# Optimization experiments

Hardware: AMD Instinct MI355X
Metric: run time of the kernel (lower is better)

Reference implementation:

```python
import jax, jax.numpy as jnp
import numpy as np

N_NODES = 50000
N_EDGES = 800000
IN_DIM = 1024
HID = 512          # hidden_channels * heads, heads=1
N_CLASSES = 6
N_GRAPHS = 8
NEG_SLOPE = 0.2    # PyG GATConv default LeakyReLU slope
EPS = 1e-16


def gat_conv(x, W, att_src, att_dst, bias, src, dst):
    """PyG GATConv with heads=1, concat=True.
    x: [N, Fin], W: [Fin, C], att_src/att_dst: [C], bias: [C],
    src/dst: [E] (edge_index[0], edge_index[1]); messages flow src -> dst.
    """
    h = x @ W                                   # [N, C]
    a_s = h @ att_src                           # [N]
    a_d = h @ att_dst                           # [N]
    e = jax.nn.leaky_relu(a_s[src] + a_d[dst], NEG_SLOPE)   # [E]
    # segment softmax over destination node
    m = jax.ops.segment_max(e, dst, num_segments=N_NODES)   # [N]
    ex = jnp.exp(e - m[dst])                                 # [E]
    denom = jax.ops.segment_sum(ex, dst, num_segments=N_NODES)  # [N]
    alpha = ex / (denom[dst] + EPS)                           # [E]
    msg = alpha[:, None] * h[src]                             # [E, C]
    out = jax.ops.segment_sum(msg, dst, num_segments=N_NODES)  # [N, C]
    return out + bias


def setup_inputs() -> dict:
    key = jax.random.key(0)
    ks = jax.random.split(key, 20)
    x = jax.random.normal(ks[0], (N_NODES, IN_DIM), dtype=jnp.float32)
    edge_index = jax.random.randint(ks[1], (2, N_EDGES), 0, N_NODES, dtype=jnp.int32)
    batch = jnp.sort(jax.random.randint(ks[2], (N_NODES,), 0, N_GRAPHS, dtype=jnp.int32))

    def glorot(k, shape):
        fan = shape[0] + shape[-1]
        return jax.random.normal(k, shape, dtype=jnp.float32) * jnp.sqrt(2.0 / fan)

    inp = {"x": x, "edge_index": edge_index, "batch": batch}
    dims = [(IN_DIM, HID), (HID, HID), (HID, HID)]
    for i, (fi, fo) in enumerate(dims, start=1):
        inp[f"W{i}"] = glorot(ks[3 * i], (fi, fo))
        inp[f"as{i}"] = glorot(ks[3 * i + 1], (fo,))
        inp[f"ad{i}"] = glorot(ks[3 * i + 2], (fo,))
        inp[f"b{i}"] = jnp.zeros((fo,), dtype=jnp.float32)
    inp["Wlin"] = glorot(ks[13], (HID, N_CLASSES))
    inp["blin"] = jnp.zeros((N_CLASSES,), dtype=jnp.float32)
    return inp


def reference(x, W1, as1, ad1, b1, W2, as2, ad2, b2, W3, as3, ad3, b3,
              Wlin, blin, edge_index, batch):
    src, dst = edge_index[0], edge_index[1]
    h = gat_conv(x, W1, as1, ad1, b1, src, dst)
    h = jax.nn.relu(h)
    h = gat_conv(h, W2, as2, ad2, b2, src, dst)
    h = jax.nn.relu(h)
    h = gat_conv(h, W3, as3, ad3, b3, src, dst)
    # global_max_pool over graphs; dropout is identity in eval mode
    pooled = jax.ops.segment_max(h, batch, num_segments=N_GRAPHS)  # [G, HID]
    return pooled @ Wlin + blin                                     # [G, num_classes]
```

## Files before the change

kernel.cpp:

```cpp
#include <hip/hip_runtime.h>
#include <cmath>

#define N_NODES 50000
#define N_EDGES 800000
#define IN_DIM 1024
#define HID 512
#define N_CLASSES 6
#define N_GRAPHS 8
#define NEG_SLOPE 0.2f
#define SCAN_BLK 256
#define N_SCAN_BLOCKS ((N_NODES + SCAN_BLK - 1) / SCAN_BLK)
#define POOL_STRIP 256
#define POOL_NBLOCKS ((N_NODES + POOL_STRIP - 1) / POOL_STRIP)

typedef _Float16 half8 __attribute__((ext_vector_type(8)));
typedef _Float16 half4 __attribute__((ext_vector_type(4)));
typedef float floatx4 __attribute__((ext_vector_type(4)));

__global__ __launch_bounds__(256) void transpose_cast_W(const float* __restrict__ W,
                                                        _Float16* __restrict__ Wt,
                                                        int K) {
    __shared__ float sh[32][33];
    const int kb = blockIdx.x * 32, nb = blockIdx.y * 32;
    const int tx = threadIdx.x & 31, ty = threadIdx.x >> 5;
#pragma unroll
    for (int i = 0; i < 32; i += 8)
        sh[ty + i][tx] = W[(size_t)(kb + ty + i) * HID + nb + tx];
    __syncthreads();
#pragma unroll
    for (int i = 0; i < 32; i += 8)
        Wt[(size_t)(nb + ty + i) * K + kb + tx] = (_Float16)sh[tx][ty + i];
}

template <typename AT>
__global__ __launch_bounds__(256) void gemm_mfma(const AT* __restrict__ A,
                                                 const _Float16* __restrict__ Bt,
                                                 _Float16* __restrict__ C,
                                                 int M, int K) {
    const int nwg = gridDim.x;
    const int bid = blockIdx.x;
    const int q = nwg >> 3, r = nwg & 7;
    const int xcd = bid & 7, local = bid >> 3;
    const int wgid = (xcd < r) ? xcd * (q + 1) + local
                               : r * (q + 1) + (xcd - r) * q + local;
    const int rowBase = (wgid >> 2) * 128;
    const int colBase = (wgid & 3) * 128;

    const int tid  = threadIdx.x;
    const int lane = tid & 63;
    const int wave = tid >> 6;
    const int wm = wave >> 1, wn = wave & 1;

    __shared__ _Float16 As[128][40];
    __shared__ _Float16 Bs[128][40];

    const int srow  = tid >> 1;
    const int shalf = (tid & 1) * 16;

    const int fr = lane & 15;
    const int kc = lane >> 4;

    floatx4 acc[4][4] = {};

    int arow = rowBase + srow; if (arow >= M) arow = M - 1;
    const AT*       aRow = A  + (size_t)arow * K + shalf;
    const _Float16* bRow = Bt + (size_t)(colBase + srow) * K + shalf;

    for (int kb = 0; kb < K; kb += 32) {
        half8* dstA = (half8*)&As[srow][shalf];
        half8* dstB = (half8*)&Bs[srow][shalf];
        if constexpr (sizeof(AT) == 4) {
            const float* ap = (const float*)aRow + kb;
            float4 af0 = *(const float4*)(ap + 0);
            float4 af1 = *(const float4*)(ap + 4);
            float4 af2 = *(const float4*)(ap + 8);
            float4 af3 = *(const float4*)(ap + 12);
            union { _Float16 h[16]; half8 v[2]; } au;
            au.h[0]  = (_Float16)af0.x; au.h[1]  = (_Float16)af0.y;
            au.h[2]  = (_Float16)af0.z; au.h[3]  = (_Float16)af0.w;
            au.h[4]  = (_Float16)af1.x; au.h[5]  = (_Float16)af1.y;
            au.h[6]  = (_Float16)af1.z; au.h[7]  = (_Float16)af1.w;
            au.h[8]  = (_Float16)af2.x; au.h[9]  = (_Float16)af2.y;
            au.h[10] = (_Float16)af2.z; au.h[11] = (_Float16)af2.w;
            au.h[12] = (_Float16)af3.x; au.h[13] = (_Float16)af3.y;
            au.h[14] = (_Float16)af3.z; au.h[15] = (_Float16)af3.w;
            dstA[0] = au.v[0]; dstA[1] = au.v[1];
        } else {
            const _Float16* ap = (const _Float16*)aRow + kb;
            half8 a0 = *(const half8*)ap;
            half8 a1 = *(const half8*)(ap + 8);
            dstA[0] = a0; dstA[1] = a1;
        }
        const _Float16* bp = bRow + kb;
        half8 b0 = *(const half8*)bp;
        half8 b1 = *(const half8*)(bp + 8);
        dstB[0] = b0; dstB[1] = b1;
        __syncthreads();

        half8 afr[4], bfr[4];
#pragma unroll
        for (int mi = 0; mi < 4; ++mi)
            afr[mi] = *(const half8*)&As[wm * 64 + mi * 16 + fr][kc * 8];
#pragma unroll
        for (int ni = 0; ni < 4; ++ni)
            bfr[ni] = *(const half8*)&Bs[wn * 64 + ni * 16 + fr][kc * 8];
#pragma unroll
        for (int mi = 0; mi < 4; ++mi)
#pragma unroll
            for (int ni = 0; ni < 4; ++ni)
                acc[mi][ni] = __builtin_amdgcn_mfma_f32_16x16x32_f16(
                    afr[mi], bfr[ni], acc[mi][ni], 0, 0, 0);
        __syncthreads();
    }

#pragma unroll
    for (int mi = 0; mi < 4; ++mi) {
#pragma unroll
        for (int ni = 0; ni < 4; ++ni) {
            int col = colBase + wn * 64 + ni * 16 + fr;
#pragma unroll
            for (int j = 0; j < 4; ++j) {
                int row = rowBase + wm * 64 + mi * 16 + kc * 4 + j;
                if (row < M) C[(size_t)row * HID + col] = (_Float16)acc[mi][ni][j];
            }
        }
    }
}

__global__ __launch_bounds__(256) void adot_kernel(const _Float16* __restrict__ h,
                                                   const float* __restrict__ att_s,
                                                   const float* __restrict__ att_d,
                                                   float* __restrict__ a_s,
                                                   float* __restrict__ a_d) {
    int wave = threadIdx.x >> 6;
    int lane = threadIdx.x & 63;
    int n = blockIdx.x * 4 + wave;
    if (n >= N_NODES) return;
    half8 hv = *(const half8*)(h + (size_t)n * HID + lane * 8);
    float4 s0 = ((const float4*)att_s)[lane * 2];
    float4 s1 = ((const float4*)att_s)[lane * 2 + 1];
    float4 d0 = ((const float4*)att_d)[lane * 2];
    float4 d1 = ((const float4*)att_d)[lane * 2 + 1];
    float hf[8];
#pragma unroll
    for (int q = 0; q < 8; ++q) hf[q] = (float)hv[q];
    float ss = hf[0]*s0.x + hf[1]*s0.y + hf[2]*s0.z + hf[3]*s0.w
             + hf[4]*s1.x + hf[5]*s1.y + hf[6]*s1.z + hf[7]*s1.w;
    float sd = hf[0]*d0.x + hf[1]*d0.y + hf[2]*d0.z + hf[3]*d0.w
             + hf[4]*d1.x + hf[5]*d1.y + hf[6]*d1.z + hf[7]*d1.w;
#pragma unroll
    for (int off = 32; off; off >>= 1) {
        ss += __shfl_down(ss, off);
        sd += __shfl_down(sd, off);
    }
    if (lane == 0) { a_s[n] = ss; a_d[n] = sd; }
}

__global__ void count_kernel(const int* __restrict__ dst, int* __restrict__ cnt) {
    int i = blockIdx.x * blockDim.x + threadIdx.x;
    if (i < N_EDGES) atomicAdd(cnt + dst[i], 1);
}

__global__ __launch_bounds__(SCAN_BLK) void scan1_kernel(const int* __restrict__ cnt,
                                                         int* __restrict__ partial,
                                                         int* __restrict__ blocksum) {
    __shared__ int tmp[SCAN_BLK];
    int t = threadIdx.x;
    int i = blockIdx.x * SCAN_BLK + t;
    int v = (i < N_NODES) ? cnt[i] : 0;
    tmp[t] = v;
    __syncthreads();
    for (int off = 1; off < SCAN_BLK; off <<= 1) {
        int u = (t >= off) ? tmp[t - off] : 0;
        __syncthreads();
        tmp[t] += u;
        __syncthreads();
    }
    if (i < N_NODES) partial[i] = tmp[t] - v;
    if (t == SCAN_BLK - 1) blocksum[blockIdx.x] = tmp[t];
}

__global__ __launch_bounds__(SCAN_BLK) void scan2_kernel(int* __restrict__ blocksum) {
    __shared__ int tmp[SCAN_BLK];
    int t = threadIdx.x;
    int v = (t < N_SCAN_BLOCKS) ? blocksum[t] : 0;
    tmp[t] = v;
    __syncthreads();
    for (int off = 1; off < SCAN_BLK; off <<= 1) {
        int u = (t >= off) ? tmp[t - off] : 0;
        __syncthreads();
        tmp[t] += u;
        __syncthreads();
    }
    if (t < N_SCAN_BLOCKS) blocksum[t] = tmp[t] - v;
}

__global__ __launch_bounds__(SCAN_BLK) void scan3_kernel(const int* __restrict__ partial,
                                                         const int* __restrict__ blocksum,
                                                         int* __restrict__ rowptr,
                                                         int* __restrict__ cursor) {
    int i = blockIdx.x * SCAN_BLK + threadIdx.x;
    if (i < N_NODES) {
        int r = partial[i] + blocksum[blockIdx.x];
        rowptr[i] = r;
        cursor[i] = r;
    }
    if (i == 0) rowptr[N_NODES] = N_EDGES;
}

__global__ void scatter_kernel(const int* __restrict__ src, const int* __restrict__ dst,
                               int* __restrict__ cursor, int* __restrict__ src_s) {
    int i = blockIdx.x * blockDim.x + threadIdx.x;
    if (i >= N_EDGES) return;
    int p = atomicAdd(cursor + dst[i], 1);
    src_s[p] = src[i];
}

__global__ __launch_bounds__(256) void aggregate_fused(const int* __restrict__ rowptr,
                                                       const int* __restrict__ src_s,
                                                       const float* __restrict__ a_s,
                                                       const float* __restrict__ a_d,
                                                       const _Float16* __restrict__ h,
                                                       const float* __restrict__ bias,
                                                       int do_relu,
                                                       _Float16* __restrict__ outx) {
    int wave = threadIdx.x >> 6;
    int lane = threadIdx.x & 63;
    int n = blockIdx.x * 4 + wave;
    if (n >= N_NODES) return;
    int beg = rowptr[n], end = rowptr[n + 1];
    float a_dn = a_d[n];
    float m = -__builtin_inff();
    float ssum = 0.f;
    float acc[8] = {};
    for (int j = beg; j < end; ++j) {
        int s = src_s[j];
        float v = a_s[s] + a_dn;
        v = v > 0.f ? v : NEG_SLOPE * v;
        float mn = fmaxf(m, v);
        float scale = __expf(m - mn);
        float p = __expf(v - mn);
        ssum = ssum * scale + p;
        m = mn;
        half8 hv = *(const half8*)(h + (size_t)s * HID + lane * 8);
#pragma unroll
        for (int q = 0; q < 8; ++q)
            acc[q] = fmaf(p, (float)hv[q], acc[q] * scale);
    }
    float inv = 1.f / (ssum + 1e-16f);
    const float4 b0 = ((const float4*)(bias + lane * 8))[0];
    const float4 b1 = ((const float4*)(bias + lane * 8))[1];
    float o[8];
    o[0] = acc[0] * inv + b0.x; o[1] = acc[1] * inv + b0.y;
    o[2] = acc[2] * inv + b0.z; o[3] = acc[3] * inv + b0.w;
    o[4] = acc[4] * inv + b1.x; o[5] = acc[5] * inv + b1.y;
    o[6] = acc[6] * inv + b1.z; o[7] = acc[7] * inv + b1.w;
    half8 ov;
#pragma unroll
    for (int q = 0; q < 8; ++q) {
        float val = do_relu ? fmaxf(o[q], 0.f) : o[q];
        ov[q] = (_Float16)val;
    }
    *(half8*)(outx + (size_t)n * HID + lane * 8) = ov;
}

__global__ __launch_bounds__(128) void pool1_kernel(const _Float16* __restrict__ X,
                                                    const int* __restrict__ batch,
                                                    float* __restrict__ partial) {
    const int t = threadIdx.x;
    const int b = blockIdx.x;
    const int n0 = b * POOL_STRIP;
    const int n1 = min(n0 + POOL_STRIP, N_NODES);
    const float NEG = -__builtin_inff();
    const float4 neg4 = make_float4(NEG, NEG, NEG, NEG);
#pragma unroll
    for (int g = 0; g < N_GRAPHS; ++g)
        ((float4*)(partial + ((size_t)b * N_GRAPHS + g) * HID))[t] = neg4;
    int gcur = batch[n0];
    float4 m = neg4;
    for (int n = n0; n < n1; ++n) {
        int g = batch[n];
        if (g != gcur) {
            ((float4*)(partial + ((size_t)b * N_GRAPHS + gcur) * HID))[t] = m;
            m = neg4;
            gcur = g;
        }
        half4 hv = *(const half4*)(X + (size_t)n * HID + t * 4);
        m.x = fmaxf(m.x, (float)hv[0]); m.y = fmaxf(m.y, (float)hv[1]);
        m.z = fmaxf(m.z, (float)hv[2]); m.w = fmaxf(m.w, (float)hv[3]);
    }
    ((float4*)(partial + ((size_t)b * N_GRAPHS + gcur) * HID))[t] = m;
}

__global__ __launch_bounds__(128) void pool2_kernel(const float* __restrict__ partial,
                                                    float* __restrict__ pooled) {
    const int g = blockIdx.x;
    const int t = threadIdx.x;
    const float NEG = -__builtin_inff();
    float4 m = make_float4(NEG, NEG, NEG, NEG);
    for (int b = 0; b < POOL_NBLOCKS; ++b) {
        float4 v = ((const float4*)(partial + ((size_t)b * N_GRAPHS + g) * HID))[t];
        m.x = fmaxf(m.x, v.x); m.y = fmaxf(m.y, v.y);
        m.z = fmaxf(m.z, v.z); m.w = fmaxf(m.w, v.w);
    }
    ((float4*)(pooled + (size_t)g * HID))[t] = m;
}

__global__ __launch_bounds__(64) void final_linear_kernel(const float* __restrict__ pooled,
                                                          const float* __restrict__ Wlin,
                                                          const float* __restrict__ blin,
                                                          float* __restrict__ out) {
    int t = threadIdx.x;
    if (t >= N_GRAPHS * N_CLASSES) return;
    int g = t / N_CLASSES, c = t % N_CLASSES;
    float s = blin[c];
    for (int k = 0; k < HID; ++k)
        s = fmaf(pooled[(size_t)g * HID + k], Wlin[(size_t)k * N_CLASSES + c], s);
    out[t] = s;
}

extern "C" void kernel_launch(void* const* d_in, const int* in_sizes, int n_in,
                              void* d_out, int out_size, void* d_ws, size_t ws_size,
                              hipStream_t stream) {
    const float* x       = (const float*)d_in[0];
    const int*   eidx    = (const int*)d_in[1];
    const int*   batch   = (const int*)d_in[2];
    const float* W[3]    = {(const float*)d_in[3], (const float*)d_in[7], (const float*)d_in[11]};
    const float* Asrc[3] = {(const float*)d_in[4], (const float*)d_in[8], (const float*)d_in[12]};
    const float* Adst[3] = {(const float*)d_in[5], (const float*)d_in[9], (const float*)d_in[13]};
    const float* Bias[3] = {(const float*)d_in[6], (const float*)d_in[10], (const float*)d_in[14]};
    const float* Wlin    = (const float*)d_in[15];
    const float* blin    = (const float*)d_in[16];
    const int* src = eidx;
    const int* dst = eidx + N_EDGES;

    float* bufH   = (float*)d_ws;
    float* bufX   = bufH + (size_t)N_NODES * HID;
    float* a_s    = bufX + (size_t)N_NODES * HID;
    float* a_d    = a_s + N_NODES;
    float* pooled = a_d + N_NODES;
    int* cnt      = (int*)(pooled + N_GRAPHS * HID);
    int* rowptr   = cnt + N_NODES;
    int* cursor   = rowptr + N_NODES + 1;
    int* partial  = cursor + N_NODES;
    int* blocksum = partial + N_NODES;
    int* src_s    = blocksum + 256;
    _Float16* Wt  = (_Float16*)(src_s + N_EDGES);
    _Float16* hH  = (_Float16*)bufH;
    _Float16* xAct= (_Float16*)bufX;

    int edge_blocks = (N_EDGES + 255) / 256;

    hipMemsetAsync(cnt, 0, N_NODES * sizeof(int), stream);
    count_kernel<<<edge_blocks, 256, 0, stream>>>(dst, cnt);
    scan1_kernel<<<N_SCAN_BLOCKS, SCAN_BLK, 0, stream>>>(cnt, partial, blocksum);
    scan2_kernel<<<1, SCAN_BLK, 0, stream>>>(blocksum);
    scan3_kernel<<<N_SCAN_BLOCKS, SCAN_BLK, 0, stream>>>(partial, blocksum, rowptr, cursor);
    scatter_kernel<<<edge_blocks, 256, 0, stream>>>(src, dst, cursor, src_s);

    const int nrow_tiles = (N_NODES + 127) / 128;
    const int gemm_blocks = nrow_tiles * (HID / 128);
    for (int l = 0; l < 3; ++l) {
        int K = (l == 0) ? IN_DIM : HID;
        dim3 tgrid(K / 32, HID / 32);
        transpose_cast_W<<<tgrid, 256, 0, stream>>>(W[l], Wt, K);
        if (l == 0)
            gemm_mfma<float><<<gemm_blocks, 256, 0, stream>>>(x, Wt, hH, N_NODES, K);
        else
            gemm_mfma<_Float16><<<gemm_blocks, 256, 0, stream>>>(xAct, Wt, hH, N_NODES, K);
        adot_kernel<<<(N_NODES + 3) / 4, 256, 0, stream>>>(hH, Asrc[l], Adst[l], a_s, a_d);
        aggregate_fused<<<(N_NODES + 3) / 4, 256, 0, stream>>>(
            rowptr, src_s, a_s, a_d, hH, Bias[l], (l < 2) ? 1 : 0, xAct);
    }

    float* pool_partial = bufH;
    pool1_kernel<<<POOL_NBLOCKS, 128, 0, stream>>>(xAct, batch, pool_partial);
    pool2_kernel<<<N_GRAPHS, 128, 0, stream>>>(pool_partial, pooled);
    final_linear_kernel<<<1, 64, 0, stream>>>(pooled, Wlin, blin, (float*)d_out);
}
```

Before: 881.2 us.

## Double-buffer GEMM shared-memory tiles with register prefetch of next K-slice

The MFMA GEMM now keeps two shared-memory buffers for the A and B tiles. Each iteration issues the global loads for the next K-slice into registers before running the MFMAs on the current buffer, then writes that slice into the other buffer. This cuts the synchronisations per iteration from two to one and lets global-memory latency overlap with compute. The cost is double the LDS footprint and more live registers, which could lower occupancy.

```diff
diff --git a/kernel.cpp b/kernel.cpp
--- a/kernel.cpp
+++ b/kernel.cpp
@@ -51,8 +51,8 @@
     const int wave = tid >> 6;
     const int wm = wave >> 1, wn = wave & 1;
 
-    __shared__ _Float16 As[128][40];
-    __shared__ _Float16 Bs[128][40];
+    __shared__ _Float16 As[2][128][40];
+    __shared__ _Float16 Bs[2][128][40];
 
     const int srow  = tid >> 1;
     const int shalf = (tid & 1) * 16;
@@ -66,16 +66,16 @@
     const AT*       aRow = A  + (size_t)arow * K + shalf;
     const _Float16* bRow = Bt + (size_t)(colBase + srow) * K + shalf;
 
-    for (int kb = 0; kb < K; kb += 32) {
-        half8* dstA = (half8*)&As[srow][shalf];
-        half8* dstB = (half8*)&Bs[srow][shalf];
+    union { _Float16 h[16]; half8 v[2]; } au;
+    half8 bv0, bv1;
+
+    auto load_tile = [&](int kb) {
         if constexpr (sizeof(AT) == 4) {
             const float* ap = (const float*)aRow + kb;
             float4 af0 = *(const float4*)(ap + 0);
             float4 af1 = *(const float4*)(ap + 4);
             float4 af2 = *(const float4*)(ap + 8);
             float4 af3 = *(const float4*)(ap + 12);
-            union { _Float16 h[16]; half8 v[2]; } au;
             au.h[0]  = (_Float16)af0.x; au.h[1]  = (_Float16)af0.y;
             au.h[2]  = (_Float16)af0.z; au.h[3]  = (_Float16)af0.w;
             au.h[4]  = (_Float16)af1.x; au.h[5]  = (_Float16)af1.y;
@@ -84,33 +84,50 @@
             au.h[10] = (_Float16)af2.z; au.h[11] = (_Float16)af2.w;
             au.h[12] = (_Float16)af3.x; au.h[13] = (_Float16)af3.y;
             au.h[14] = (_Float16)af3.z; au.h[15] = (_Float16)af3.w;
-            dstA[0] = au.v[0]; dstA[1] = au.v[1];
         } else {
             const _Float16* ap = (const _Float16*)aRow + kb;
-            half8 a0 = *(const half8*)ap;
-            half8 a1 = *(const half8*)(ap + 8);
-            dstA[0] = a0; dstA[1] = a1;
+            au.v[0] = *(const half8*)ap;
+            au.v[1] = *(const half8*)(ap + 8);
         }
         const _Float16* bp = bRow + kb;
-        half8 b0 = *(const half8*)bp;
-        half8 b1 = *(const half8*)(bp + 8);
-        dstB[0] = b0; dstB[1] = b1;
-        __syncthreads();
+        bv0 = *(const half8*)bp;
+        bv1 = *(const half8*)(bp + 8);
+    };
+    auto store_tile = [&](int buf) {
+        half8* dstA = (half8*)&As[buf][srow][shalf];
+        half8* dstB = (half8*)&Bs[buf][srow][shalf];
+        dstA[0] = au.v[0]; dstA[1] = au.v[1];
+        dstB[0] = bv0;     dstB[1] = bv1;
+    };
+
+    load_tile(0);
+    store_tile(0);
+    __syncthreads();
+
+    int cur = 0;
+    for (int kb = 0; kb < K; kb += 32) {
+        const bool has_next = (kb + 32) < K;
+        if (has_next) load_tile(kb + 32);
 
         half8 afr[4], bfr[4];
 #pragma unroll
         for (int mi = 0; mi < 4; ++mi)
-            afr[mi] = *(const half8*)&As[wm * 64 + mi * 16 + fr][kc * 8];
+            afr[mi] = *(const half8*)&As[cur][wm * 64 + mi * 16 + fr][kc * 8];
 #pragma unroll
         for (int ni = 0; ni < 4; ++ni)
-            bfr[ni] = *(const half8*)&Bs[wn * 64 + ni * 16 + fr][kc * 8];
+            bfr[ni] = *(const half8*)&Bs[cur][wn * 64 + ni * 16 + fr][kc * 8];
 #pragma unroll
         for (int mi = 0; mi < 4; ++mi)
 #pragma unroll
             for (int ni = 0; ni < 4; ++ni)
                 acc[mi][ni] = __builtin_amdgcn_mfma_f32_16x16x32_f16(
                     afr[mi], bfr[ni], acc[mi][ni], 0, 0, 0);
-        __syncthreads();
+
+        if (has_next) {
+            store_tile(cur ^ 1);
+            __syncthreads();
+            cur ^= 1;
+        }
     }
 
 #pragma unroll
```

Result: slower. 940.1 us (+6.7%).

## Use direct global-to-LDS loads with swizzled 64-wide K tiles in GEMM

Applied to the files above, without the earlier changes.

Adds a separate pass that casts x to fp16 up front, so one fp16 GEMM kernel serves all three layers. The GEMM now fills LDS with global_load_lds 16-byte copies into an XOR-swizzled 128x64 layout, doubling the K step and halving the number of barriers. This removes the register round trip and the in-loop fp32 conversion. The cost is an extra full read and write of x, and the workspace offsets are rearranged to hold the fp16 copy.

```diff
diff --git a/kernel.cpp b/kernel.cpp
--- a/kernel.cpp
+++ b/kernel.cpp
@@ -17,6 +17,28 @@
 typedef _Float16 half4 __attribute__((ext_vector_type(4)));
 typedef float floatx4 __attribute__((ext_vector_type(4)));
 
+typedef const __attribute__((address_space(1))) void* gas_ptr;
+typedef __attribute__((address_space(3))) void* las_ptr;
+#define GLOAD16(gp, lp) \
+    __builtin_amdgcn_global_load_lds((gas_ptr)(gp), (las_ptr)(lp), 16, 0, 0)
+
+__global__ __launch_bounds__(256) void cast_x_f16(const float* __restrict__ x,
+                                                  _Float16* __restrict__ x16) {
+    const size_t TOT = (size_t)N_NODES * IN_DIM;
+    size_t i = ((size_t)blockIdx.x * blockDim.x + threadIdx.x) * 8;
+    const size_t step = (size_t)gridDim.x * blockDim.x * 8;
+    for (; i < TOT; i += step) {
+        float4 f0 = *(const float4*)(x + i);
+        float4 f1 = *(const float4*)(x + i + 4);
+        half8 o;
+        o[0] = (_Float16)f0.x; o[1] = (_Float16)f0.y;
+        o[2] = (_Float16)f0.z; o[3] = (_Float16)f0.w;
+        o[4] = (_Float16)f1.x; o[5] = (_Float16)f1.y;
+        o[6] = (_Float16)f1.z; o[7] = (_Float16)f1.w;
+        *(half8*)(x16 + i) = o;
+    }
+}
+
 __global__ __launch_bounds__(256) void transpose_cast_W(const float* __restrict__ W,
                                                         _Float16* __restrict__ Wt,
                                                         int K) {
@@ -32,11 +54,10 @@
         Wt[(size_t)(nb + ty + i) * K + kb + tx] = (_Float16)sh[tx][ty + i];
 }
 
-template <typename AT>
-__global__ __launch_bounds__(256) void gemm_mfma(const AT* __restrict__ A,
-                                                 const _Float16* __restrict__ Bt,
-                                                 _Float16* __restrict__ C,
-                                                 int M, int K) {
+__global__ __launch_bounds__(256) void gemm_mfma_f16(const _Float16* __restrict__ A,
+                                                     const _Float16* __restrict__ Bt,
+                                                     _Float16* __restrict__ C,
+                                                     int M, int K) {
     const int nwg = gridDim.x;
     const int bid = blockIdx.x;
     const int q = nwg >> 3, r = nwg & 7;
@@ -51,65 +72,60 @@
     const int wave = tid >> 6;
     const int wm = wave >> 1, wn = wave & 1;
 
-    __shared__ _Float16 As[128][40];
-    __shared__ _Float16 Bs[128][40];
-
-    const int srow  = tid >> 1;
-    const int shalf = (tid & 1) * 16;
+    __shared__ __align__(16) _Float16 As[128 * 64];
+    __shared__ __align__(16) _Float16 Bs[128 * 64];
 
     const int fr = lane & 15;
     const int kc = lane >> 4;
 
     floatx4 acc[4][4] = {};
 
-    int arow = rowBase + srow; if (arow >= M) arow = M - 1;
-    const AT*       aRow = A  + (size_t)arow * K + shalf;
-    const _Float16* bRow = Bt + (size_t)(colBase + srow) * K + shalf;
-
-    for (int kb = 0; kb < K; kb += 32) {
-        half8* dstA = (half8*)&As[srow][shalf];
-        half8* dstB = (half8*)&Bs[srow][shalf];
-        if constexpr (sizeof(AT) == 4) {
-            const float* ap = (const float*)aRow + kb;
-            float4 af0 = *(const float4*)(ap + 0);
-            float4 af1 = *(const float4*)(ap + 4);
-            float4 af2 = *(const float4*)(ap + 8);
-            float4 af3 = *(const float4*)(ap + 12);
-            union { _Float16 h[16]; half8 v[2]; } au;
-            au.h[0]  = (_Float16)af0.x; au.h[1]  = (_Float16)af0.y;
-            au.h[2]  = (_Float16)af0.z; au.h[3]  = (_Float16)af0.w;
-            au.h[4]  = (_Float16)af1.x; au.h[5]  = (_Float16)af1.y;
-            au.h[6]  = (_Float16)af1.z; au.h[7]  = (_Float16)af1.w;
-            au.h[8]  = (_Float16)af2.x; au.h[9]  = (_Float16)af2.y;
-            au.h[10] = (_Float16)af2.z; au.h[11] = (_Float16)af2.w;
-            au.h[12] = (_Float16)af3.x; au.h[13] = (_Float16)af3.y;
-            au.h[14] = (_Float16)af3.z; au.h[15] = (_Float16)af3.w;
-            dstA[0] = au.v[0]; dstA[1] = au.v[1];
-        } else {
-            const _Float16* ap = (const _Float16*)aRow + kb;
-            half8 a0 = *(const half8*)ap;
-            half8 a1 = *(const half8*)(ap + 8);
-            dstA[0] = a0; dstA[1] = a1;
+    const int lrow   = lane >> 3;
+    const int gchunk = ((lane & 7) ^ lrow) * 8;
+    const _Float16* aS[4];
+    const _Float16* bS[4];
+    _Float16* aD[4];
+    _Float16* bD[4];
+#pragma unroll
+    for (int i = 0; i < 4; ++i) {
+        int rr = wave * 32 + i * 8;
+        int ar = rowBase + rr + lrow; if (ar > M - 1) ar = M - 1;
+        aS[i] = A  + (size_t)ar * K + gchunk;
+        bS[i] = Bt + (size_t)(colBase + rr + lrow) * K + gchunk;
+        aD[i] = As + rr * 64;
+        bD[i] = Bs + rr * 64;
+    }
+
+    const int cp0 = ((kc)     ^ (fr & 7)) * 8;
+    const int cp1 = ((4 + kc) ^ (fr & 7)) * 8;
+    const int aro = (wm * 64 + fr) * 64;
+    const int bro = (wn * 64 + fr) * 64;
+
+    for (int kb = 0; kb < K; kb += 64) {
+#pragma unroll
+        for (int i = 0; i < 4; ++i) {
+            GLOAD16(aS[i] + kb, aD[i]);
+            GLOAD16(bS[i] + kb, bD[i]);
         }
-        const _Float16* bp = bRow + kb;
-        half8 b0 = *(const half8*)bp;
-        half8 b1 = *(const half8*)(bp + 8);
-        dstB[0] = b0; dstB[1] = b1;
-        __syncthreads();
-
-        half8 afr[4], bfr[4];
-#pragma unroll
-        for (int mi = 0; mi < 4; ++mi)
-            afr[mi] = *(const half8*)&As[wm * 64 + mi * 16 + fr][kc * 8];
-#pragma unroll
-        for (int ni = 0; ni < 4; ++ni)
-            bfr[ni] = *(const half8*)&Bs[wn * 64 + ni * 16 + fr][kc * 8];
-#pragma unroll
-        for (int mi = 0; mi < 4; ++mi)
+        __syncthreads();
+
+#pragma unroll
+        for (int kks = 0; kks < 2; ++kks) {
+            const int cp = kks ? cp1 : cp0;
+            half8 afr[4], bfr[4];
+#pragma unroll
+            for (int mi = 0; mi < 4; ++mi)
+                afr[mi] = *(const half8*)&As[aro + mi * 1024 + cp];
 #pragma unroll
             for (int ni = 0; ni < 4; ++ni)
-                acc[mi][ni] = __builtin_amdgcn_mfma_f32_16x16x32_f16(
-                    afr[mi], bfr[ni], acc[mi][ni], 0, 0, 0);
+                bfr[ni] = *(const half8*)&Bs[bro + ni * 1024 + cp];
+#pragma unroll
+            for (int mi = 0; mi < 4; ++mi)
+#pragma unroll
+                for (int ni = 0; ni < 4; ++ni)
+                    acc[mi][ni] = __builtin_amdgcn_mfma_f32_16x16x32_f16(
+                        afr[mi], bfr[ni], acc[mi][ni], 0, 0, 0);
+        }
         __syncthreads();
     }
 
@@ -334,9 +350,11 @@
     const int* src = eidx;
     const int* dst = eidx + N_EDGES;
 
-    float* bufH   = (float*)d_ws;
-    float* bufX   = bufH + (size_t)N_NODES * HID;
-    float* a_s    = bufX + (size_t)N_NODES * HID;
+    float* wsf    = (float*)d_ws;
+    _Float16* x16 = (_Float16*)wsf;
+    _Float16* hH  = (_Float16*)(wsf + 25600000);
+    _Float16* xAct= (_Float16*)(wsf + 25600000 + 12800000);
+    float* a_s    = wsf + 25600000 + 12800000 + 12800000;
     float* a_d    = a_s + N_NODES;
     float* pooled = a_d + N_NODES;
     int* cnt      = (int*)(pooled + N_GRAPHS * HID);
@@ -346,8 +364,6 @@
     int* blocksum = partial + N_NODES;
     int* src_s    = blocksum + 256;
     _Float16* Wt  = (_Float16*)(src_s + N_EDGES);
-    _Float16* hH  = (_Float16*)bufH;
-    _Float16* xAct= (_Float16*)bufX;
 
     int edge_blocks = (N_EDGES + 255) / 256;
 
@@ -358,22 +374,22 @@
     scan3_kernel<<<N_SCAN_BLOCKS, SCAN_BLK, 0, stream>>>(partial, blocksum, rowptr, cursor);
     scatter_kernel<<<edge_blocks, 256, 0, stream>>>(src, dst, cursor, src_s);
 
+    cast_x_f16<<<2048, 256, 0, stream>>>(x, x16);
+
     const int nrow_tiles = (N_NODES + 127) / 128;
     const int gemm_blocks = nrow_tiles * (HID / 128);
     for (int l = 0; l < 3; ++l) {
         int K = (l == 0) ? IN_DIM : HID;
         dim3 tgrid(K / 32, HID / 32);
         transpose_cast_W<<<tgrid, 256, 0, stream>>>(W[l], Wt, K);
-        if (l == 0)
-            gemm_mfma<float><<<gemm_blocks, 256, 0, stream>>>(x, Wt, hH, N_NODES, K);
-        else
-            gemm_mfma<_Float16><<<gemm_blocks, 256, 0, stream>>>(xAct, Wt, hH, N_NODES, K);
+        const _Float16* Ain = (l == 0) ? x16 : xAct;
+        gemm_mfma_f16<<<gemm_blocks, 256, 0, stream>>>(Ain, Wt, hH, N_NODES, K);
         adot_kernel<<<(N_NODES + 3) / 4, 256, 0, stream>>>(hH, Asrc[l], Adst[l], a_s, a_d);
         aggregate_fused<<<(N_NODES + 3) / 4, 256, 0, stream>>>(
             rowptr, src_s, a_s, a_d, hH, Bias[l], (l < 2) ? 1 : 0, xAct);
     }
 
-    float* pool_partial = bufH;
+    float* pool_partial = (float*)x16;
     pool1_kernel<<<POOL_NBLOCKS, 128, 0, stream>>>(xAct, batch, pool_partial);
     pool2_kernel<<<N_GRAPHS, 128, 0, stream>>>(pool_partial, pooled);
     final_linear_kernel<<<1, 64, 0, stream>>>(pooled, Wlin, blin, (float*)d_out);
```

After: 840.0 us. -4.7%, faster.
